# Performance work log

Measured on AMD Instinct MI355X. Metric: run time of the kernel, lower is better.

Reference implementation:

```python
import jax, jax.numpy as jnp
import numpy as np

BN_EPS = 1e-5

def setup_inputs() -> dict:
    key = jax.random.key(0)
    ks = jax.random.split(key, 5)
    B, C, H, W = 4, 64, 64, 64
    s = 1.0 / np.sqrt(C)
    return {
        "x": jax.random.normal(ks[0], (B, C, H, W), dtype=jnp.float32),
        "Wk": jax.random.normal(ks[1], (C, C), dtype=jnp.float32) * s,
        "Wq": jax.random.normal(ks[2], (C, C), dtype=jnp.float32) * s,
        "Wv": jax.random.normal(ks[3], (C, C), dtype=jnp.float32) * s,
        "W2": jax.random.normal(ks[4], (C, C), dtype=jnp.float32) * s,
        "gamma": jnp.ones((C,), dtype=jnp.float32),
        "beta": jnp.zeros((C,), dtype=jnp.float32),
        "running_mean": jnp.zeros((C,), dtype=jnp.float32),
        "running_var": jnp.ones((C,), dtype=jnp.float32),
    }

def reference(x, Wk, Wq, Wv, W2, gamma, beta, running_mean, running_var):
    B, C, H, W = x.shape
    N = H * W
    xf = x.reshape(B, C, N)                      # flatten spatial -> (B,C,N)
    # 1x1 convs (no bias) == channel matmuls
    k = jnp.einsum('oc,bcn->bon', Wk, xf)        # (B,C,N)
    q = jnp.einsum('oc,bcn->bon', Wq, xf)
    v = jnp.einsum('oc,bcn->bon', Wv, xf)
    # scores[b,n,m] = sum_c k[b,c,n] * q[b,c,m]  (note: no 1/sqrt(d) scaling, as in source)
    scores = jnp.einsum('bcn,bcm->bnm', k, q)    # (B,N,N)
    p = jax.nn.softmax(scores, axis=2)
    # att[b,c,n] = sum_m p[b,n,m] * v[b,c,m]
    att = jnp.einsum('bnm,bcm->bcn', p, v)       # (B,C,N)
    y = jnp.einsum('oc,bcn->bon', W2, att)       # 1x1 conv
    inv = gamma / jnp.sqrt(running_var + BN_EPS)
    y = y * inv[None, :, None] + (beta - running_mean * inv)[None, :, None]
    y = jax.nn.relu(y)
    return y.reshape(B, C, H, W) + x
```

## Files before the change

kernel.cpp:

```cpp
#include <hip/hip_runtime.h>
#include <math.h>

#define CH   64
#define NTOT 4096
#define NB   4

typedef short  short4v  __attribute__((ext_vector_type(4)));
typedef short  short8v  __attribute__((ext_vector_type(8)));
typedef float  floatx4  __attribute__((ext_vector_type(4)));

static __device__ __forceinline__ short f2bf(float f) {
    union { float f; unsigned int u; } v; v.f = f;
    unsigned int r = v.u + 0x7FFFu + ((v.u >> 16) & 1u);
    return (short)(r >> 16);
}

__global__ __launch_bounds__(256) void qkv_proj(
    const float* __restrict__ x,
    const float* __restrict__ Wk, const float* __restrict__ Wq,
    const float* __restrict__ Wv,
    short* __restrict__ kT, short* __restrict__ qT, short* __restrict__ vg)
{
    __shared__ __align__(16) float xs [64][68];
    __shared__ __align__(16) float wkT[64][68];
    __shared__ __align__(16) float wqT[64][68];
    __shared__ __align__(16) float wvT[64][68];

    const int tid = threadIdx.x;
    const int b  = blockIdx.x >> 6;
    const int n0 = (blockIdx.x & 63) * 64;
    const float* xb = x + (size_t)b * CH * NTOT;

    for (int i = tid; i < 64 * 64; i += 256) {
        int c = i >> 6, n = i & 63;
        xs[c][n] = xb[(size_t)c * NTOT + n0 + n];
    }
    for (int i = tid; i < 64 * 64; i += 256) {
        int o = i >> 6, c = i & 63;
        wkT[c][o] = Wk[i];
        wqT[c][o] = Wq[i];
        wvT[c][o] = Wv[i];
    }
    __syncthreads();

    const int to = tid >> 4, tn = tid & 15;
    const int ob = to * 4, nb = tn * 4;
    float ak[4][4] = {}, aq[4][4] = {}, av[4][4] = {};

    for (int c = 0; c < 64; ++c) {
        float4 xv = *(const float4*)&xs [c][nb];
        float4 k4 = *(const float4*)&wkT[c][ob];
        float4 q4 = *(const float4*)&wqT[c][ob];
        float4 v4 = *(const float4*)&wvT[c][ob];
        float xa[4] = {xv.x, xv.y, xv.z, xv.w};
        float ka[4] = {k4.x, k4.y, k4.z, k4.w};
        float qa[4] = {q4.x, q4.y, q4.z, q4.w};
        float va[4] = {v4.x, v4.y, v4.z, v4.w};
        #pragma unroll
        for (int i = 0; i < 4; ++i)
            #pragma unroll
            for (int j = 0; j < 4; ++j) {
                ak[i][j] += ka[i] * xa[j];
                aq[i][j] += qa[i] * xa[j];
                av[i][j] += va[i] * xa[j];
            }
    }

    #pragma unroll
    for (int j = 0; j < 4; ++j) {
        size_t row = (size_t)(b << 12) + n0 + nb + j;
        short4v kk = { f2bf(ak[0][j]), f2bf(ak[1][j]), f2bf(ak[2][j]), f2bf(ak[3][j]) };
        short4v qq = { f2bf(aq[0][j]), f2bf(aq[1][j]), f2bf(aq[2][j]), f2bf(aq[3][j]) };
        *(short4v*)&kT[row * 64 + ob] = kk;
        *(short4v*)&qT[row * 64 + ob] = qq;
    }
    #pragma unroll
    for (int i = 0; i < 4; ++i) {
        short4v vv = { f2bf(av[i][0]), f2bf(av[i][1]), f2bf(av[i][2]), f2bf(av[i][3]) };
        *(short4v*)&vg[(((size_t)(b << 6) + ob + i) << 12) + n0 + nb] = vv;
    }
}

__global__ __launch_bounds__(512) void fused_attn(
    const short* __restrict__ kT, const short* __restrict__ qT,
    const short* __restrict__ vg,
    const float* __restrict__ W2,
    const float* __restrict__ gamma, const float* __restrict__ beta,
    const float* __restrict__ rmean, const float* __restrict__ rvar,
    const float* __restrict__ x, float* __restrict__ out)
{
    __shared__ __align__(16) short smem[32256];

    const int tid = threadIdx.x;
    const int w    = tid >> 6;
    const int l    = tid & 63;
    const int g    = l >> 4;
    const int ln   = l & 15;
    const int half = w >> 2;
    const int wq   = w & 3;

    const int bid = blockIdx.x;
    const int xcd = bid & 7, idx = bid >> 3;
    const int b    = xcd >> 1;
    const int nblk = ((xcd & 1) << 5) | idx;
    const int n0   = nblk << 6;

    const short* kTb = kT + ((size_t)(b << 12) + n0) * 64;
    const short* qTb = qT + ((size_t)b << 12) * 64;
    const short* vb  = vg + ((size_t)(b << 6) << 12);

    short* const kTs = smem;
    short* const qH  = smem + 4608  + half * 4608;
    short* const vH  = smem + 13824 + half * 4608;
    short* const PsW = smem + 23040 + w * 1152;

    {
        int r = tid >> 3, c8 = (tid & 7) << 3;
        *(short8v*)&kTs[r * 72 + c8] = *(const short8v*)&kTb[r * 64 + c8];
    }
    __syncthreads();

    short8v bS0 = *(const short8v*)&kTs[((wq << 4) + ln) * 72 + (g << 3)];
    short8v bS1 = *(const short8v*)&kTs[((wq << 4) + ln) * 72 + 32 + (g << 3)];

    float mrun = -1e30f;
    float lrun = 0.f;
    floatx4 acc_o[4];
    #pragma unroll
    for (int ct = 0; ct < 4; ++ct) acc_o[ct] = (floatx4){0.f, 0.f, 0.f, 0.f};

    const int m0h = half << 11;
    const int i0 = tid & 255, i1 = (tid & 255) + 256;

    short8v pf[4];
    pf[0] = *(const short8v*)&qTb[(size_t)(m0h + (i0 >> 3)) * 64 + ((i0 & 7) << 3)];
    pf[1] = *(const short8v*)&qTb[(size_t)(m0h + (i1 >> 3)) * 64 + ((i1 & 7) << 3)];
    pf[2] = *(const short8v*)&vb[(size_t)(i0 >> 3) * 4096 + m0h + ((i0 & 7) << 3)];
    pf[3] = *(const short8v*)&vb[(size_t)(i1 >> 3) * 4096 + m0h + ((i1 & 7) << 3)];

    for (int t = 0; t < 32; ++t) {
        __syncthreads();
        *(short8v*)&qH[(i0 >> 3) * 72 + ((i0 & 7) << 3)] = pf[0];
        *(short8v*)&qH[(i1 >> 3) * 72 + ((i1 & 7) << 3)] = pf[1];
        *(short8v*)&vH[(i0 >> 3) * 72 + ((i0 & 7) << 3)] = pf[2];
        *(short8v*)&vH[(i1 >> 3) * 72 + ((i1 & 7) << 3)] = pf[3];
        __syncthreads();
        if (t < 31) {
            int m1 = m0h + ((t + 1) << 6);
            pf[0] = *(const short8v*)&qTb[(size_t)(m1 + (i0 >> 3)) * 64 + ((i0 & 7) << 3)];
            pf[1] = *(const short8v*)&qTb[(size_t)(m1 + (i1 >> 3)) * 64 + ((i1 & 7) << 3)];
            pf[2] = *(const short8v*)&vb[(size_t)(i0 >> 3) * 4096 + m1 + ((i0 & 7) << 3)];
            pf[3] = *(const short8v*)&vb[(size_t)(i1 >> 3) * 4096 + m1 + ((i1 & 7) << 3)];
        }

        floatx4 sacc[4];
        #pragma unroll
        for (int mt = 0; mt < 4; ++mt) {
            short8v a0 = *(const short8v*)&qH[((mt << 4) + ln) * 72 + (g << 3)];
            short8v a1 = *(const short8v*)&qH[((mt << 4) + ln) * 72 + 32 + (g << 3)];
            floatx4 acc = (floatx4){0.f, 0.f, 0.f, 0.f};
            acc = __builtin_amdgcn_mfma_f32_16x16x32_bf16(a0, bS0, acc, 0, 0, 0);
            acc = __builtin_amdgcn_mfma_f32_16x16x32_bf16(a1, bS1, acc, 0, 0, 0);
            sacc[mt] = acc;
        }

        float mx = sacc[0][0];
        #pragma unroll
        for (int mt = 0; mt < 4; ++mt)
            #pragma unroll
            for (int r = 0; r < 4; ++r) mx = fmaxf(mx, sacc[mt][r]);
        mx = fmaxf(mx, __shfl_xor(mx, 16));
        mx = fmaxf(mx, __shfl_xor(mx, 32));

        float mnew = fmaxf(mrun, mx);
        float fs = __expf(mrun - mnew);
        mrun = mnew;

        float s = 0.f;
        #pragma unroll
        for (int mt = 0; mt < 4; ++mt) {
            float p0 = __expf(sacc[mt][0] - mnew);
            float p1 = __expf(sacc[mt][1] - mnew);
            float p2 = __expf(sacc[mt][2] - mnew);
            float p3 = __expf(sacc[mt][3] - mnew);
            s += (p0 + p1) + (p2 + p3);
            short4v p4 = { f2bf(p0), f2bf(p1), f2bf(p2), f2bf(p3) };
            *(short4v*)&PsW[ln * 72 + (mt << 4) + (g << 2)] = p4;
        }
        s += __shfl_xor(s, 16);
        s += __shfl_xor(s, 32);
        lrun = lrun * fs + s;

        #pragma unroll
        for (int ct = 0; ct < 4; ++ct) {
            acc_o[ct][0] *= fs; acc_o[ct][1] *= fs;
            acc_o[ct][2] *= fs; acc_o[ct][3] *= fs;
        }

        short8v bp0 = *(const short8v*)&PsW[ln * 72 + (g << 3)];
        short8v bp1 = *(const short8v*)&PsW[ln * 72 + 32 + (g << 3)];
        #pragma unroll
        for (int ct = 0; ct < 4; ++ct) {
            short8v a0 = *(const short8v*)&vH[((ct << 4) + ln) * 72 + (g << 3)];
            short8v a1 = *(const short8v*)&vH[((ct << 4) + ln) * 72 + 32 + (g << 3)];
            acc_o[ct] = __builtin_amdgcn_mfma_f32_16x16x32_bf16(a0, bp0, acc_o[ct], 0, 0, 0);
            acc_o[ct] = __builtin_amdgcn_mfma_f32_16x16x32_bf16(a1, bp1, acc_o[ct], 0, 0, 0);
        }
    }

    float* mb = (float*)smem;
    if (g == 0) {
        mb[(((half << 2) | wq) << 4) + ln]       = mrun;
        mb[128 + (((half << 2) | wq) << 4) + ln] = lrun;
    }
    __syncthreads();

    float m0v = mb[(wq << 4) + ln];
    float m1v = mb[64 + (wq << 4) + ln];
    float l0v = mb[128 + (wq << 4) + ln];
    float l1v = mb[192 + (wq << 4) + ln];
    float mm = fmaxf(m0v, m1v);
    float s0 = __expf(m0v - mm), s1 = __expf(m1v - mm);

    float* xbuf = (float*)(smem + 4608);
    if (half == 1) {
        #pragma unroll
        for (int ct = 0; ct < 4; ++ct) {
            float4 w4 = make_float4(acc_o[ct][0] * s1, acc_o[ct][1] * s1,
                                    acc_o[ct][2] * s1, acc_o[ct][3] * s1);
            *(float4*)&xbuf[((wq << 4) + ln) * 68 + (ct << 4) + (g << 2)] = w4;
        }
    }
    __syncthreads();
    if (half == 0) {
        float linv = 1.0f / (l0v * s0 + l1v * s1);
        #pragma unroll
        for (int ct = 0; ct < 4; ++ct) {
            float4 x1 = *(const float4*)&xbuf[((wq << 4) + ln) * 68 + (ct << 4) + (g << 2)];
            float xa[4] = {x1.x, x1.y, x1.z, x1.w};
            short4v a4 = { f2bf((acc_o[ct][0] * s0 + xa[0]) * linv),
                           f2bf((acc_o[ct][1] * s0 + xa[1]) * linv),
                           f2bf((acc_o[ct][2] * s0 + xa[2]) * linv),
                           f2bf((acc_o[ct][3] * s0 + xa[3]) * linv) };
            *(short4v*)&PsW[ln * 72 + (ct << 4) + (g << 2)] = a4;
        }
    }
    __syncthreads();

    for (int i = tid; i < 1024; i += 512) {
        int r = i >> 4, c4 = (i & 15) << 2;
        float4 wv = *(const float4*)&W2[(r << 6) + c4];
        short4v s4 = { f2bf(wv.x), f2bf(wv.y), f2bf(wv.z), f2bf(wv.w) };
        *(short4v*)&smem[r * 72 + c4] = s4;
    }
    __syncthreads();

    const int sq  = w & 3;
    const int ob2 = (w >> 2) << 1;
    const short* PsQ = smem + 23040 + sq * 1152;
    short8v bA0 = *(const short8v*)&PsQ[ln * 72 + (g << 3)];
    short8v bA1 = *(const short8v*)&PsQ[ln * 72 + 32 + (g << 3)];
    const int nq = n0 + (sq << 4) + ln;
    #pragma unroll
    for (int oi = 0; oi < 2; ++oi) {
        int ot = ob2 + oi;
        short8v a0 = *(const short8v*)&smem[((ot << 4) + ln) * 72 + (g << 3)];
        short8v a1 = *(const short8v*)&smem[((ot << 4) + ln) * 72 + 32 + (g << 3)];
        floatx4 acc = (floatx4){0.f, 0.f, 0.f, 0.f};
        acc = __builtin_amdgcn_mfma_f32_16x16x32_bf16(a0, bA0, acc, 0, 0, 0);
        acc = __builtin_amdgcn_mfma_f32_16x16x32_bf16(a1, bA1, acc, 0, 0, 0);
        int o0 = (ot << 4) + (g << 2);
        float4 gm = *(const float4*)&gamma[o0];
        float4 bt = *(const float4*)&beta [o0];
        float4 rm = *(const float4*)&rmean[o0];
        float4 rv = *(const float4*)&rvar [o0];
        float gma[4] = {gm.x, gm.y, gm.z, gm.w};
        float bta[4] = {bt.x, bt.y, bt.z, bt.w};
        float rma[4] = {rm.x, rm.y, rm.z, rm.w};
        float rva[4] = {rv.x, rv.y, rv.z, rv.w};
        #pragma unroll
        for (int r = 0; r < 4; ++r) {
            float inv  = gma[r] * rsqrtf(rva[r] + 1e-5f);
            float bias = bta[r] - rma[r] * inv;
            size_t ga = (((size_t)(b << 6) + o0 + r) << 12) + nq;
            out[ga] = fmaxf(acc[r] * inv + bias, 0.f) + x[ga];
        }
    }
}

extern "C" void kernel_launch(void* const* d_in, const int* in_sizes, int n_in,
                              void* d_out, int out_size, void* d_ws, size_t ws_size,
                              hipStream_t stream)
{
    const float* x     = (const float*)d_in[0];
    const float* Wk    = (const float*)d_in[1];
    const float* Wq    = (const float*)d_in[2];
    const float* Wv    = (const float*)d_in[3];
    const float* W2    = (const float*)d_in[4];
    const float* gamma = (const float*)d_in[5];
    const float* beta  = (const float*)d_in[6];
    const float* rmean = (const float*)d_in[7];
    const float* rvar  = (const float*)d_in[8];
    float* out = (float*)d_out;

    const size_t plane = (size_t)NB * NTOT * CH;
    short* kT = (short*)d_ws;
    short* qT = kT + plane;
    short* vv = qT + plane;

    qkv_proj  <<<dim3(256), dim3(256), 0, stream>>>(x, Wk, Wq, Wv, kT, qT, vv);
    fused_attn<<<dim3(256), dim3(512), 0, stream>>>(kT, qT, vv, W2, gamma, beta,
                                                    rmean, rvar, x, out);
}
```

Before: 60.38 us.

## Split attention across key chunks with separate merge kernel (flash-decoding style)

Replaces the single fused attention kernel (256 blocks of 512 threads, two key halves merged in shared memory) with a split-K scheme. 1024 blocks of 256 threads each process a quarter of the keys and write partial outputs plus running max and sum to workspace. A new merge kernel then combines the four partials, applies W2, BN, ReLU and the residual. This raises the block count to fill more CUs, at the cost of an extra launch and roughly 16MB of fp32 partial-output traffic through global memory.

```diff
diff --git a/kernel.cpp b/kernel.cpp
--- a/kernel.cpp
+++ b/kernel.cpp
@@ -81,47 +81,47 @@
     }
 }
 
-__global__ __launch_bounds__(512) void fused_attn(
+__global__ __launch_bounds__(256) void attn_partial(
     const short* __restrict__ kT, const short* __restrict__ qT,
     const short* __restrict__ vg,
-    const float* __restrict__ W2,
-    const float* __restrict__ gamma, const float* __restrict__ beta,
-    const float* __restrict__ rmean, const float* __restrict__ rvar,
-    const float* __restrict__ x, float* __restrict__ out)
+    float* __restrict__ opart, float* __restrict__ mlpart)
 {
-    __shared__ __align__(16) short smem[32256];
+    __shared__ __align__(16) short smem[18432];
 
     const int tid = threadIdx.x;
-    const int w    = tid >> 6;
-    const int l    = tid & 63;
-    const int g    = l >> 4;
-    const int ln   = l & 15;
-    const int half = w >> 2;
-    const int wq   = w & 3;
-
-    const int bid = blockIdx.x;
-    const int xcd = bid & 7, idx = bid >> 3;
-    const int b    = xcd >> 1;
-    const int nblk = ((xcd & 1) << 5) | idx;
-    const int n0   = nblk << 6;
+    const int w  = tid >> 6;
+    const int l  = tid & 63;
+    const int g  = l >> 4;
+    const int ln = l & 15;
+
+    const int bid  = blockIdx.x;
+    const int xcd  = bid & 7, grp = bid >> 3;
+    const int bk   = (xcd << 1) | (grp >> 6);
+    const int b    = bk >> 2;
+    const int kc   = bk & 3;
+    const int qblk = grp & 63;
+    const int n0   = qblk << 6;
+    const int part = (b << 8) | (kc << 6) | qblk;
+    const int kbase = kc << 10;
 
     const short* kTb = kT + ((size_t)(b << 12) + n0) * 64;
     const short* qTb = qT + ((size_t)b << 12) * 64;
     const short* vb  = vg + ((size_t)(b << 6) << 12);
 
     short* const kTs = smem;
-    short* const qH  = smem + 4608  + half * 4608;
-    short* const vH  = smem + 13824 + half * 4608;
-    short* const PsW = smem + 23040 + w * 1152;
+    short* const qS  = smem + 4608;
+    short* const vS  = smem + 9216;
+    short* const PsW = smem + 13824 + w * 1152;
 
     {
-        int r = tid >> 3, c8 = (tid & 7) << 3;
-        *(short8v*)&kTs[r * 72 + c8] = *(const short8v*)&kTb[r * 64 + c8];
-    }
-    __syncthreads();
-
-    short8v bS0 = *(const short8v*)&kTs[((wq << 4) + ln) * 72 + (g << 3)];
-    short8v bS1 = *(const short8v*)&kTs[((wq << 4) + ln) * 72 + 32 + (g << 3)];
+        int r0 = tid >> 3, c8 = (tid & 7) << 3;
+        *(short8v*)&kTs[r0 * 72 + c8]        = *(const short8v*)&kTb[r0 * 64 + c8];
+        *(short8v*)&kTs[(r0 + 32) * 72 + c8] = *(const short8v*)&kTb[(r0 + 32) * 64 + c8];
+    }
+    __syncthreads();
+
+    short8v bS0 = *(const short8v*)&kTs[((w << 4) + ln) * 72 + (g << 3)];
+    short8v bS1 = *(const short8v*)&kTs[((w << 4) + ln) * 72 + 32 + (g << 3)];
 
     float mrun = -1e30f;
     float lrun = 0.f;
@@ -129,24 +129,23 @@
     #pragma unroll
     for (int ct = 0; ct < 4; ++ct) acc_o[ct] = (floatx4){0.f, 0.f, 0.f, 0.f};
 
-    const int m0h = half << 11;
-    const int i0 = tid & 255, i1 = (tid & 255) + 256;
+    const int i0 = tid, i1 = tid + 256;
 
     short8v pf[4];
-    pf[0] = *(const short8v*)&qTb[(size_t)(m0h + (i0 >> 3)) * 64 + ((i0 & 7) << 3)];
-    pf[1] = *(const short8v*)&qTb[(size_t)(m0h + (i1 >> 3)) * 64 + ((i1 & 7) << 3)];
-    pf[2] = *(const short8v*)&vb[(size_t)(i0 >> 3) * 4096 + m0h + ((i0 & 7) << 3)];
-    pf[3] = *(const short8v*)&vb[(size_t)(i1 >> 3) * 4096 + m0h + ((i1 & 7) << 3)];
-
-    for (int t = 0; t < 32; ++t) {
+    pf[0] = *(const short8v*)&qTb[(size_t)(kbase + (i0 >> 3)) * 64 + ((i0 & 7) << 3)];
+    pf[1] = *(const short8v*)&qTb[(size_t)(kbase + (i1 >> 3)) * 64 + ((i1 & 7) << 3)];
+    pf[2] = *(const short8v*)&vb[(size_t)(i0 >> 3) * 4096 + kbase + ((i0 & 7) << 3)];
+    pf[3] = *(const short8v*)&vb[(size_t)(i1 >> 3) * 4096 + kbase + ((i1 & 7) << 3)];
+
+    for (int t = 0; t < 16; ++t) {
         __syncthreads();
-        *(short8v*)&qH[(i0 >> 3) * 72 + ((i0 & 7) << 3)] = pf[0];
-        *(short8v*)&qH[(i1 >> 3) * 72 + ((i1 & 7) << 3)] = pf[1];
-        *(short8v*)&vH[(i0 >> 3) * 72 + ((i0 & 7) << 3)] = pf[2];
-        *(short8v*)&vH[(i1 >> 3) * 72 + ((i1 & 7) << 3)] = pf[3];
+        *(short8v*)&qS[(i0 >> 3) * 72 + ((i0 & 7) << 3)] = pf[0];
+        *(short8v*)&qS[(i1 >> 3) * 72 + ((i1 & 7) << 3)] = pf[1];
+        *(short8v*)&vS[(i0 >> 3) * 72 + ((i0 & 7) << 3)] = pf[2];
+        *(short8v*)&vS[(i1 >> 3) * 72 + ((i1 & 7) << 3)] = pf[3];
         __syncthreads();
-        if (t < 31) {
-            int m1 = m0h + ((t + 1) << 6);
+        if (t < 15) {
+            int m1 = kbase + ((t + 1) << 6);
             pf[0] = *(const short8v*)&qTb[(size_t)(m1 + (i0 >> 3)) * 64 + ((i0 & 7) << 3)];
             pf[1] = *(const short8v*)&qTb[(size_t)(m1 + (i1 >> 3)) * 64 + ((i1 & 7) << 3)];
             pf[2] = *(const short8v*)&vb[(size_t)(i0 >> 3) * 4096 + m1 + ((i0 & 7) << 3)];
@@ -156,8 +155,8 @@
         floatx4 sacc[4];
         #pragma unroll
         for (int mt = 0; mt < 4; ++mt) {
-            short8v a0 = *(const short8v*)&qH[((mt << 4) + ln) * 72 + (g << 3)];
-            short8v a1 = *(const short8v*)&qH[((mt << 4) + ln) * 72 + 32 + (g << 3)];
+            short8v a0 = *(const short8v*)&qS[((mt << 4) + ln) * 72 + (g << 3)];
+            short8v a1 = *(const short8v*)&qS[((mt << 4) + ln) * 72 + 32 + (g << 3)];
             floatx4 acc = (floatx4){0.f, 0.f, 0.f, 0.f};
             acc = __builtin_amdgcn_mfma_f32_16x16x32_bf16(a0, bS0, acc, 0, 0, 0);
             acc = __builtin_amdgcn_mfma_f32_16x16x32_bf16(a1, bS1, acc, 0, 0, 0);
@@ -201,71 +200,113 @@
         short8v bp1 = *(const short8v*)&PsW[ln * 72 + 32 + (g << 3)];
         #pragma unroll
         for (int ct = 0; ct < 4; ++ct) {
-            short8v a0 = *(const short8v*)&vH[((ct << 4) + ln) * 72 + (g << 3)];
-            short8v a1 = *(const short8v*)&vH[((ct << 4) + ln) * 72 + 32 + (g << 3)];
+            short8v a0 = *(const short8v*)&vS[((ct << 4) + ln) * 72 + (g << 3)];
+            short8v a1 = *(const short8v*)&vS[((ct << 4) + ln) * 72 + 32 + (g << 3)];
             acc_o[ct] = __builtin_amdgcn_mfma_f32_16x16x32_bf16(a0, bp0, acc_o[ct], 0, 0, 0);
             acc_o[ct] = __builtin_amdgcn_mfma_f32_16x16x32_bf16(a1, bp1, acc_o[ct], 0, 0, 0);
         }
     }
 
-    float* mb = (float*)smem;
+    __syncthreads();
+    float* xp = (float*)(smem + 4608);
+    #pragma unroll
+    for (int ct = 0; ct < 4; ++ct)
+        #pragma unroll
+        for (int r = 0; r < 4; ++r)
+            xp[((w << 4) + ln) * 68 + (ct << 4) + (g << 2) + r] = acc_o[ct][r];
     if (g == 0) {
-        mb[(((half << 2) | wq) << 4) + ln]       = mrun;
-        mb[128 + (((half << 2) | wq) << 4) + ln] = lrun;
-    }
-    __syncthreads();
-
-    float m0v = mb[(wq << 4) + ln];
-    float m1v = mb[64 + (wq << 4) + ln];
-    float l0v = mb[128 + (wq << 4) + ln];
-    float l1v = mb[192 + (wq << 4) + ln];
-    float mm = fmaxf(m0v, m1v);
-    float s0 = __expf(m0v - mm), s1 = __expf(m1v - mm);
-
-    float* xbuf = (float*)(smem + 4608);
-    if (half == 1) {
-        #pragma unroll
-        for (int ct = 0; ct < 4; ++ct) {
-            float4 w4 = make_float4(acc_o[ct][0] * s1, acc_o[ct][1] * s1,
-                                    acc_o[ct][2] * s1, acc_o[ct][3] * s1);
-            *(float4*)&xbuf[((wq << 4) + ln) * 68 + (ct << 4) + (g << 2)] = w4;
-        }
-    }
-    __syncthreads();
-    if (half == 0) {
-        float linv = 1.0f / (l0v * s0 + l1v * s1);
-        #pragma unroll
-        for (int ct = 0; ct < 4; ++ct) {
-            float4 x1 = *(const float4*)&xbuf[((wq << 4) + ln) * 68 + (ct << 4) + (g << 2)];
-            float xa[4] = {x1.x, x1.y, x1.z, x1.w};
-            short4v a4 = { f2bf((acc_o[ct][0] * s0 + xa[0]) * linv),
-                           f2bf((acc_o[ct][1] * s0 + xa[1]) * linv),
-                           f2bf((acc_o[ct][2] * s0 + xa[2]) * linv),
-                           f2bf((acc_o[ct][3] * s0 + xa[3]) * linv) };
-            *(short4v*)&PsW[ln * 72 + (ct << 4) + (g << 2)] = a4;
-        }
-    }
-    __syncthreads();
-
-    for (int i = tid; i < 1024; i += 512) {
+        mlpart[(size_t)part * 128 + (w << 4) + ln]      = mrun;
+        mlpart[(size_t)part * 128 + 64 + (w << 4) + ln] = lrun;
+    }
+    __syncthreads();
+    {
+        int q = tid >> 2, c16 = (tid & 3) << 4;
+        float* Ob = opart + (size_t)part * 4096 + q * 64 + c16;
+        #pragma unroll
+        for (int i = 0; i < 4; ++i)
+            *(float4*)&Ob[i << 2] = *(const float4*)&xp[q * 68 + c16 + (i << 2)];
+    }
+}
+
+__global__ __launch_bounds__(256) void attn_merge(
+    const float* __restrict__ opart, const float* __restrict__ mlpart,
+    const float* __restrict__ W2,
+    const float* __restrict__ gamma, const float* __restrict__ beta,
+    const float* __restrict__ rmean, const float* __restrict__ rvar,
+    const float* __restrict__ x, float* __restrict__ out)
+{
+    __shared__ __align__(16) short attL[64 * 72];
+    __shared__ __align__(16) short w2s [64 * 72];
+    __shared__ float wgt[4][64];
+    __shared__ float linv[64];
+
+    const int tid = threadIdx.x;
+    const int w  = tid >> 6;
+    const int l  = tid & 63;
+    const int g  = l >> 4;
+    const int ln = l & 15;
+
+    const int b    = blockIdx.x >> 6;
+    const int qblk = blockIdx.x & 63;
+    const int n0   = qblk << 6;
+    const int part0 = (b << 8) | qblk;
+
+    if (tid < 64) {
+        float m0 = mlpart[(size_t)(part0)        * 128 + tid];
+        float m1 = mlpart[(size_t)(part0 + 64)   * 128 + tid];
+        float m2 = mlpart[(size_t)(part0 + 128)  * 128 + tid];
+        float m3 = mlpart[(size_t)(part0 + 192)  * 128 + tid];
+        float l0 = mlpart[(size_t)(part0)        * 128 + 64 + tid];
+        float l1 = mlpart[(size_t)(part0 + 64)   * 128 + 64 + tid];
+        float l2 = mlpart[(size_t)(part0 + 128)  * 128 + 64 + tid];
+        float l3 = mlpart[(size_t)(part0 + 192)  * 128 + 64 + tid];
+        float mm = fmaxf(fmaxf(m0, m1), fmaxf(m2, m3));
+        float w0 = __expf(m0 - mm), w1 = __expf(m1 - mm);
+        float w2 = __expf(m2 - mm), w3 = __expf(m3 - mm);
+        wgt[0][tid] = w0; wgt[1][tid] = w1; wgt[2][tid] = w2; wgt[3][tid] = w3;
+        linv[tid] = 1.0f / (w0 * l0 + w1 * l1 + w2 * l2 + w3 * l3);
+    }
+    for (int i = tid; i < 1024; i += 256) {
         int r = i >> 4, c4 = (i & 15) << 2;
         float4 wv = *(const float4*)&W2[(r << 6) + c4];
         short4v s4 = { f2bf(wv.x), f2bf(wv.y), f2bf(wv.z), f2bf(wv.w) };
-        *(short4v*)&smem[r * 72 + c4] = s4;
-    }
-    __syncthreads();
-
-    const int sq  = w & 3;
-    const int ob2 = (w >> 2) << 1;
-    const short* PsQ = smem + 23040 + sq * 1152;
-    short8v bA0 = *(const short8v*)&PsQ[ln * 72 + (g << 3)];
-    short8v bA1 = *(const short8v*)&PsQ[ln * 72 + 32 + (g << 3)];
-    const int nq = n0 + (sq << 4) + ln;
-    #pragma unroll
-    for (int oi = 0; oi < 2; ++oi) {
-        int ot = ob2 + oi;
-        short8v a0 = *(const short8v*)&smem[((ot << 4) + ln) * 72 + (g << 3)];
-        short8v a1 = *(const short8v*)&smem[((ot << 4) + ln) * 72 + 32 + (g << 3)];
+        *(short4v*)&w2s[r * 72 + c4] = s4;
+    }
+    __syncthreads();
+
+    {
+        int q = tid >> 2, c16 = (tid & 3) << 4;
+        float a[16] = {};
+        #pragma unroll
+        for (int kc = 0; kc < 4; ++kc) {
+            float wk = wgt[kc][q];
+            const float* Ob = opart + (size_t)(part0 + (kc << 6)) * 4096 + q * 64 + c16;
+            #pragma unroll
+            for (int i = 0; i < 4; ++i) {
+                float4 o4 = *(const float4*)&Ob[i << 2];
+                a[(i << 2) + 0] += wk * o4.x;
+                a[(i << 2) + 1] += wk * o4.y;
+                a[(i << 2) + 2] += wk * o4.z;
+                a[(i << 2) + 3] += wk * o4.w;
+            }
+        }
+        float li = linv[q];
+        #pragma unroll
+        for (int i = 0; i < 4; ++i) {
+            short4v s4 = { f2bf(a[(i << 2) + 0] * li), f2bf(a[(i << 2) + 1] * li),
+                           f2bf(a[(i << 2) + 2] * li), f2bf(a[(i << 2) + 3] * li) };
+            *(short4v*)&attL[q * 72 + c16 + (i << 2)] = s4;
+        }
+    }
+    __syncthreads();
+
+    short8v bA0 = *(const short8v*)&attL[((w << 4) + ln) * 72 + (g << 3)];
+    short8v bA1 = *(const short8v*)&attL[((w << 4) + ln) * 72 + 32 + (g << 3)];
+    const int nq = n0 + (w << 4) + ln;
+    #pragma unroll
+    for (int ot = 0; ot < 4; ++ot) {
+        short8v a0 = *(const short8v*)&w2s[((ot << 4) + ln) * 72 + (g << 3)];
+        short8v a1 = *(const short8v*)&w2s[((ot << 4) + ln) * 72 + 32 + (g << 3)];
         floatx4 acc = (floatx4){0.f, 0.f, 0.f, 0.f};
         acc = __builtin_amdgcn_mfma_f32_16x16x32_bf16(a0, bA0, acc, 0, 0, 0);
         acc = __builtin_amdgcn_mfma_f32_16x16x32_bf16(a1, bA1, acc, 0, 0, 0);
@@ -307,8 +348,11 @@
     short* kT = (short*)d_ws;
     short* qT = kT + plane;
     short* vv = qT + plane;
-
-    qkv_proj  <<<dim3(256), dim3(256), 0, stream>>>(x, Wk, Wq, Wv, kT, qT, vv);
-    fused_attn<<<dim3(256), dim3(512), 0, stream>>>(kT, qT, vv, W2, gamma, beta,
-                                                    rmean, rvar, x, out);
-}
+    float* opart  = (float*)(vv + plane);
+    float* mlpart = opart + (size_t)1024 * 4096;
+
+    qkv_proj    <<<dim3(256),  dim3(256), 0, stream>>>(x, Wk, Wq, Wv, kT, qT, vv);
+    attn_partial<<<dim3(1024), dim3(256), 0, stream>>>(kT, qT, vv, opart, mlpart);
+    attn_merge  <<<dim3(256),  dim3(256), 0, stream>>>(opart, mlpart, W2, gamma, beta,
+                                                       rmean, rvar, x, out);
+}
```

New measurement: 67.58 us. 1.12x slower.
